# Kernel optimization log

Measured on AMD Instinct MI355X. Metric: run time of the kernel, lower is better.

Reference implementation:

```python
import jax, jax.numpy as jnp
import numpy as np

EPS = 1e-8

def _normalize(a):
    return a / jnp.clip(jnp.linalg.norm(a, axis=-1, keepdims=True), EPS)

def _cosine(a, b):
    # pairwise cosine similarity: [Na, d] x [Nb, d] -> [Na, Nb]
    return _normalize(a) @ _normalize(b).T

def setup_inputs() -> dict:
    key = jax.random.key(0)
    n, k, q, d = 100, 5, 75, 4096
    x = jax.random.normal(key, (n * (k + q), d), dtype=jnp.float32)
    tao = jnp.full((1,), 10.0, dtype=jnp.float32)
    return {"x": x, "tao": tao, "n": n, "k": k, "q": q}

def reference(x, tao, n, k, q):
    d = x.shape[-1]
    x = x.reshape(n, k + q, d)
    support = x[:, :k]                      # [n, k, d]
    query = x[:, k:].reshape(n * q, d)      # [NQ, d]
    NQ = n * q
    proto = support.mean(axis=1)            # [n, d]

    pre_sim = _cosine(query, proto)         # [NQ, n]
    pre_label = jnp.argmax(pre_sim, axis=1) # [NQ]

    # vectorized per-class masked softmax aggregation (replaces Python loop)
    cls_ids = jnp.arange(n)
    mask = pre_label[None, :] == cls_ids[:, None]            # [n, NQ]
    logits_q = jnp.where(mask, pre_sim.T, -jnp.inf)          # [n, NQ]
    proto_n = _normalize(proto)
    self_sim = jnp.sum(proto_n * proto_n, axis=-1)           # [n], cosine(proto, proto)
    logits = jnp.concatenate([logits_q, self_sim[:, None]], axis=1)  # [n, NQ+1]
    w = jax.nn.softmax(logits, axis=1)                       # [n, NQ+1]
    adapted_proto = w[:, :NQ] @ query + w[:, NQ:] * proto    # [n, d]

    sim = _cosine(query, adapted_proto)                      # [NQ, n]
    return tao.reshape(()) * sim
```

## Files before the change

kernel.cpp:

```cpp
#include <hip/hip_runtime.h>
#include <hip/hip_bf16.h>
#include <math.h>

#define NQUERY 7500
#define NCLS   100
#define DIM    4096
#define KQ     75
#define KSUP   5
#define RPC    80
#define MPAD   7552
#define NPAD   112
#define CAPQ   256
#define RCAP   2048
#define EPSF   1e-8f
#define SELEM  845824

typedef __attribute__((ext_vector_type(8))) short bf16x8;
typedef __attribute__((ext_vector_type(4))) short s16x4;
typedef __attribute__((ext_vector_type(4))) float f32x4;

__device__ __forceinline__ int xrow_of_query(int j) {
    return (j / KQ) * RPC + KSUP + (j % KQ);
}
__device__ __forceinline__ short bf16t(float x) {
    union { float f; unsigned u; } v; v.f = x;
    return (short)(v.u >> 16);
}

__device__ __forceinline__ size_t tile_off(int nt, int lm, int i) {
    return (((size_t)(nt * 128 + (i >> 5)) * 4 + ((i >> 3) & 3)) * 16 + lm) * 8 + (i & 7);
}

__global__ __launch_bounds__(256) void k_proto(const float* __restrict__ x,
        float* __restrict__ proto, short* __restrict__ Phi, float* __restrict__ es,
        double* __restrict__ pninv) {
    const int c = blockIdx.x, t = threadIdx.x;
    const int nt = c >> 4, lm = c & 15;
    if (c >= NCLS) {
        for (int g = t; g < 512; g += 256) {
            const int kstep = g >> 2, kq = g & 3;
            size_t o = (((size_t)(nt * 128 + kstep) * 4 + kq) * 16 + lm) * 8;
            bf16x8 z = {0,0,0,0,0,0,0,0};
            *(bf16x8*)(Phi + o) = z;
        }
        if (t == 0) es[c] = 0.f;
        return;
    }
    __shared__ double red[4];
    __shared__ float s_inv;
    const float* b0 = x + (size_t)(c * RPC) * DIM;
    float v[16];
    double ssq = 0.0;
#pragma unroll
    for (int p = 0; p < 4; ++p) {
        const int i = p * 1024 + t * 4;
        f32x4 s = {0.f, 0.f, 0.f, 0.f};
#pragma unroll
        for (int r = 0; r < KSUP; ++r)
            s += *(const f32x4*)(b0 + (size_t)r * DIM + i);
        s = s / 5.0f;
        *(f32x4*)&v[p*4] = s;
        *(f32x4*)(proto + (size_t)c*DIM + i) = s;
        ssq += (double)s[0]*s[0] + (double)s[1]*s[1]
             + (double)s[2]*s[2] + (double)s[3]*s[3];
    }
    for (int o = 32; o; o >>= 1) ssq += __shfl_down(ssq, o);
    if ((t & 63) == 0) red[t >> 6] = ssq;
    __syncthreads();
    if (t == 0) {
        double dtot = red[0] + red[1] + red[2] + red[3];
        pninv[c] = 1.0 / sqrt(dtot);
        float tot = (float)dtot;
        float inv = 1.f / fmaxf(sqrtf(tot), EPSF);
        s_inv = inv;
        es[c] = expf(tot * inv * inv);
    }
    __syncthreads();
    const float inv = s_inv;
#pragma unroll
    for (int p = 0; p < 4; ++p) {
        const int i = p * 1024 + t * 4;
        s16x4 h;
#pragma unroll
        for (int e = 0; e < 4; ++e) h[e] = bf16t(v[p*4+e] * inv);
        *(s16x4*)(Phi + tile_off(nt, lm, i)) = h;
    }
}

template<int TNKS, bool SSQ>
__global__ __launch_bounds__(256, 3) void k_gemm(const float* __restrict__ x,
        const short* __restrict__ Bt, float* __restrict__ Sd, float* __restrict__ nq2) {
    constexpr int KST = 128 / TNKS;
    const int bx = blockIdx.x, kz = blockIdx.y;
    const int w = threadIdx.x >> 6, lane = threadIdx.x & 63;
    const int lm = lane & 15, kq = lane >> 4;
    const int mp = bx * 4 + w;
    const int mt0 = mp * 2, mt1 = mt0 + 1;
    const int j0 = mt0 * 16 + lm, j1 = mt1 * 16 + lm;
    const int jc0 = j0 < NQUERY ? j0 : NQUERY - 1;
    const int jc1 = j1 < NQUERY ? j1 : NQUERY - 1;
    const float* pa0 = x + (size_t)xrow_of_query(jc0) * DIM + kq * 8;
    const float* pa1 = x + (size_t)xrow_of_query(jc1) * DIM + kq * 8;
    const short* pb = Bt + (lane << 3);
    const int ks0 = kz * KST;

    f32x4 acc0[7], acc1[7];
#pragma unroll
    for (int nt = 0; nt < 7; ++nt) {
        acc0[nt] = (f32x4){0.f,0.f,0.f,0.f};
        acc1[nt] = (f32x4){0.f,0.f,0.f,0.f};
    }
    float ssq0 = 0.f, ssq1 = 0.f;

    f32x4 a00 = *(const f32x4*)(pa0 + (size_t)ks0 * 32);
    f32x4 a01 = *(const f32x4*)(pa0 + (size_t)ks0 * 32 + 4);
    f32x4 a10 = *(const f32x4*)(pa1 + (size_t)ks0 * 32);
    f32x4 a11 = *(const f32x4*)(pa1 + (size_t)ks0 * 32 + 4);

#pragma unroll 1
    for (int s = 0; s < KST; ++s) {
        const int ks = ks0 + s;
        bf16x8 bh[7];
#pragma unroll
        for (int nt = 0; nt < 7; ++nt)
            bh[nt] = *(const bf16x8*)(pb + (((size_t)(nt * 128 + ks)) << 9));
        f32x4 n00, n01, n10, n11;
        if (s + 1 < KST) {
            n00 = *(const f32x4*)(pa0 + (size_t)(ks + 1) * 32);
            n01 = *(const f32x4*)(pa0 + (size_t)(ks + 1) * 32 + 4);
            n10 = *(const f32x4*)(pa1 + (size_t)(ks + 1) * 32);
            n11 = *(const f32x4*)(pa1 + (size_t)(ks + 1) * 32 + 4);
        }
        float f0[8] = {a00[0],a00[1],a00[2],a00[3],a01[0],a01[1],a01[2],a01[3]};
        float f1[8] = {a10[0],a10[1],a10[2],a10[3],a11[0],a11[1],a11[2],a11[3]};
        bf16x8 ah0, ah1;
#pragma unroll
        for (int e = 0; e < 8; ++e) {
            if (SSQ) { ssq0 += f0[e] * f0[e]; ssq1 += f1[e] * f1[e]; }
            ah0[e] = bf16t(f0[e]);
            ah1[e] = bf16t(f1[e]);
        }
#pragma unroll
        for (int nt = 0; nt < 7; ++nt) {
            acc0[nt] = __builtin_amdgcn_mfma_f32_16x16x32_bf16(ah0, bh[nt], acc0[nt], 0, 0, 0);
            acc1[nt] = __builtin_amdgcn_mfma_f32_16x16x32_bf16(ah1, bh[nt], acc1[nt], 0, 0, 0);
        }
        a00 = n00; a01 = n01; a10 = n10; a11 = n11;
    }

    if (SSQ) {
        ssq0 += __shfl_xor(ssq0, 16); ssq0 += __shfl_xor(ssq0, 32);
        ssq1 += __shfl_xor(ssq1, 16); ssq1 += __shfl_xor(ssq1, 32);
        if (kq == 0) {
            if (j0 < NQUERY) atomicAdd(&nq2[j0], ssq0);
            if (j1 < NQUERY) atomicAdd(&nq2[j1], ssq1);
        }
    }
    float* s0 = Sd + (size_t)(mt0 * 16) * NPAD;
    float* s1 = Sd + (size_t)(mt1 * 16) * NPAD;
#pragma unroll
    for (int nt = 0; nt < 7; ++nt)
#pragma unroll
        for (int r = 0; r < 4; ++r) {
            atomicAdd(&s0[(size_t)(kq * 4 + r) * NPAD + nt * 16 + lm], acc0[nt][r]);
            atomicAdd(&s1[(size_t)(kq * 4 + r) * NPAD + nt * 16 + lm], acc1[nt][r]);
        }
}

__global__ __launch_bounds__(256) void k_argmax(const float* __restrict__ S,
        const float* __restrict__ nq2, float* __restrict__ coef, float* __restrict__ invq,
        int* __restrict__ pos, int* __restrict__ ccnt, int* __restrict__ cls_list,
        int* __restrict__ rcnt, int* __restrict__ rlist) {
    const int j = blockIdx.x * 256 + threadIdx.x;
    if (j >= NQUERY) return;
    const float* row = S + (size_t)j * NPAD;
    float m1 = -1e30f, m2 = -1e30f;
    int i1 = 0, i2 = 0;
    for (int c = 0; c < NCLS; ++c) {
        float v = row[c];
        if (v > m1) { m2 = m1; i2 = i1; m1 = v; i1 = c; }
        else if (v > m2) { m2 = v; i2 = c; }
    }
    const float inv = 1.f / fmaxf(sqrtf(nq2[j]), EPSF);
    invq[j] = inv;
    coef[j] = expf(m1 * inv);
    const int p = atomicAdd(&ccnt[i1], 1);
    if (p < CAPQ) { cls_list[i1 * CAPQ + p] = j; pos[j] = p; }
    else pos[j] = -1;
    if ((m1 - m2) * inv < 5e-4f) {
        int rp = atomicAdd(rcnt, 1);
        if (rp < RCAP) rlist[rp] = j | (i1 << 13) | (i2 << 20);
    }
}

__global__ __launch_bounds__(256) void k_refine(const float* __restrict__ x,
        const float* __restrict__ proto, const double* __restrict__ pninv,
        const float* __restrict__ S, const float* __restrict__ invq,
        float* __restrict__ coef, const int* __restrict__ pos,
        int* __restrict__ ccnt, int* __restrict__ cls_list,
        const int* __restrict__ rcnt, const int* __restrict__ rlist) {
    const int cnt = min(*rcnt, RCAP);
    const int t = threadIdx.x;
    __shared__ double red1[4], red2[4];
    for (int e = blockIdx.x; e < cnt; e += gridDim.x) {
        const int pk = rlist[e];
        const int j = pk & 8191, c1 = (pk >> 13) & 127, c2 = (pk >> 20) & 127;
        const float* xq = x + (size_t)xrow_of_query(j) * DIM;
        const float* p1 = proto + (size_t)c1 * DIM;
        const float* p2 = proto + (size_t)c2 * DIM;
        double d1 = 0.0, d2 = 0.0;
        for (int i = t; i < DIM; i += 256) {
            const double qv = (double)xq[i];
            d1 += (double)p1[i] * qv;
            d2 += (double)p2[i] * qv;
        }
        for (int o = 32; o; o >>= 1) { d1 += __shfl_down(d1, o); d2 += __shfl_down(d2, o); }
        if ((t & 63) == 0) { red1[t >> 6] = d1; red2[t >> 6] = d2; }
        __syncthreads();
        if (t == 0) {
            const double cos1 = (red1[0]+red1[1]+red1[2]+red1[3]) * pninv[c1];
            const double cos2 = (red2[0]+red2[1]+red2[2]+red2[3]) * pninv[c2];
            const int win = (cos2 > cos1 || (cos2 == cos1 && c2 < c1)) ? c2 : c1;
            if (win != c1) {
                coef[j] = expf(S[(size_t)j * NPAD + win] * invq[j]);
                const int pj = pos[j];
                if (pj >= 0) cls_list[c1 * CAPQ + pj] = -1;
                const int np = atomicAdd(&ccnt[c2], 1);
                if (np < CAPQ) cls_list[c2 * CAPQ + np] = j;
            }
        }
        __syncthreads();
    }
}

__global__ __launch_bounds__(128) void k_adapt(const float* __restrict__ x,
        const float* __restrict__ coef, const int* __restrict__ cls_cnt,
        const int* __restrict__ cls_list, float* __restrict__ APpart) {
    __shared__ int   s_j[CAPQ];
    __shared__ float s_cf[CAPQ];
    const int cx = blockIdx.x, c = blockIdx.y, sl = blockIdx.z;
    const int n = min(cls_cnt[c], CAPQ);
    for (int e = threadIdx.x; e < n; e += 128) {
        const int j = cls_list[c * CAPQ + e];
        s_j[e] = j;
        s_cf[e] = (j >= 0) ? coef[j] : 0.f;
    }
    __syncthreads();
    const int i0 = cx * 512 + threadIdx.x * 4;
    f32x4 acc = {0.f, 0.f, 0.f, 0.f};
    for (int e = sl; e < n; e += 4) {
        const int j = s_j[e];
        if (j >= 0) {
            const float cf = s_cf[e];
            const f32x4 v = *(const f32x4*)(x + (size_t)xrow_of_query(j) * DIM + i0);
            acc += v * cf;
        }
    }
    *(f32x4*)(APpart + (size_t)sl * NCLS * DIM + (size_t)c * DIM + i0) = acc;
}

__global__ __launch_bounds__(256) void k_apnorm(const float* __restrict__ APpart,
        const float* __restrict__ proto, const float* __restrict__ es,
        short* __restrict__ APhi) {
    const int c = blockIdx.x, t = threadIdx.x;
    const int nt = c >> 4, lm = c & 15;
    if (c >= NCLS) {
        for (int g = t; g < 512; g += 256) {
            const int kstep = g >> 2, kq = g & 3;
            size_t o = (((size_t)(nt * 128 + kstep) * 4 + kq) * 16 + lm) * 8;
            bf16x8 z = {0,0,0,0,0,0,0,0};
            *(bf16x8*)(APhi + o) = z;
        }
        return;
    }
    __shared__ float red[4];
    __shared__ float s_inv;
    const float e0 = es[c];
    float v[16];
    float ssq = 0.f;
#pragma unroll
    for (int p = 0; p < 4; ++p) {
        const int i = p * 1024 + t * 4;
        f32x4 s = {0.f, 0.f, 0.f, 0.f};
#pragma unroll
        for (int sl = 0; sl < 4; ++sl)
            s += *(const f32x4*)(APpart + (size_t)sl * NCLS * DIM + (size_t)c * DIM + i);
        f32x4 pr = *(const f32x4*)(proto + (size_t)c*DIM + i);
        s += pr * e0;
        *(f32x4*)&v[p*4] = s;
        ssq += s[0]*s[0] + s[1]*s[1] + s[2]*s[2] + s[3]*s[3];
    }
    for (int o = 32; o; o >>= 1) ssq += __shfl_down(ssq, o);
    if ((t & 63) == 0) red[t >> 6] = ssq;
    __syncthreads();
    if (t == 0) {
        float tot = red[0] + red[1] + red[2] + red[3];
        s_inv = 1.f / fmaxf(sqrtf(tot), EPSF);
    }
    __syncthreads();
    const float inv = s_inv;
#pragma unroll
    for (int p = 0; p < 4; ++p) {
        const int i = p * 1024 + t * 4;
        s16x4 h;
#pragma unroll
        for (int e = 0; e < 4; ++e) h[e] = bf16t(v[p*4+e] * inv);
        *(s16x4*)(APhi + tile_off(nt, lm, i)) = h;
    }
}

__global__ __launch_bounds__(256) void k_scale(const float* __restrict__ Ored,
        const float* __restrict__ invq, const float* __restrict__ tao,
        float* __restrict__ out) {
    const int idx = blockIdx.x * 256 + threadIdx.x;
    if (idx >= NQUERY * 25) return;
    const int j = idx / 25, c4 = (idx % 25) * 4;
    const f32x4 s = *(const f32x4*)(Ored + (size_t)j * NPAD + c4);
    const float sc = tao[0] * invq[j];
    *(f32x4*)(out + (size_t)j * NCLS + c4) = s * sc;
}

#define OFF_RCNT   0u
#define OFF_CCNT   256u
#define OFF_NQ2    1792u
#define ZERO_BYTES 32768u
#define OFF_ES     32768u
#define OFF_INVQ   33280u
#define OFF_POS    63488u
#define OFF_COEF   93696u
#define OFF_RLIST  123904u
#define OFF_CLIST  132096u
#define OFF_PNINV  234496u
#define OFF_PROTO  235520u
#define OFF_PHI    1873920u
#define OFF_APHI   2791424u
#define OFF_SRED   3708928u
#define OFF_ORED   7092224u
#define OFF_APPART 10475520u

extern "C" void kernel_launch(void* const* d_in, const int* in_sizes, int n_in,
                              void* d_out, int out_size, void* d_ws, size_t ws_size,
                              hipStream_t stream) {
    const float* x   = (const float*)d_in[0];
    const float* tao = (const float*)d_in[1];
    char* ws = (char*)d_ws;

    int*    rcnt    = (int*)   (ws + OFF_RCNT);
    int*    ccnt    = (int*)   (ws + OFF_CCNT);
    float*  nq2     = (float*) (ws + OFF_NQ2);
    float*  es      = (float*) (ws + OFF_ES);
    float*  invq    = (float*) (ws + OFF_INVQ);
    int*    pos     = (int*)   (ws + OFF_POS);
    float*  coef    = (float*) (ws + OFF_COEF);
    int*    rlist   = (int*)   (ws + OFF_RLIST);
    int*    clist   = (int*)   (ws + OFF_CLIST);
    double* pninv   = (double*)(ws + OFF_PNINV);
    float*  proto   = (float*) (ws + OFF_PROTO);
    short*  Phi     = (short*) (ws + OFF_PHI);
    short*  APhi    = (short*) (ws + OFF_APHI);
    float*  Sred    = (float*) (ws + OFF_SRED);
    float*  Ored    = (float*) (ws + OFF_ORED);
    float*  APpart  = (float*) (ws + OFF_APPART);

    hipMemsetAsync(ws, 0, ZERO_BYTES, stream);
    hipMemsetAsync(ws + OFF_SRED, 0, 2u * 3383296u, stream);

    k_proto <<<NPAD, 256, 0, stream>>>(x, proto, Phi, es, pninv);
    k_gemm<16, true><<<dim3(59, 16), 256, 0, stream>>>(x, Phi, Sred, nq2);
    k_argmax <<<30, 256, 0, stream>>>(Sred, nq2, coef, invq, pos, ccnt, clist, rcnt, rlist);
    k_refine <<<512, 256, 0, stream>>>(x, proto, pninv, Sred, invq, coef, pos, ccnt, clist, rcnt, rlist);
    k_adapt  <<<dim3(8, NCLS, 4), 128, 0, stream>>>(x, coef, ccnt, clist, APpart);
    k_apnorm <<<NPAD, 256, 0, stream>>>(APpart, proto, es, APhi);
    k_gemm<16, false><<<dim3(59, 16), 256, 0, stream>>>(x, APhi, Ored, nq2);
    k_scale  <<<733, 256, 0, stream>>>(Ored, invq, tao, (float*)d_out);
}
```

Before: 358.6 us.

## Fuse all stages into one cooperative persistent kernel with grid syncs

Replaces the eight separate kernel launches with a single cooperative megakernel whose stages are separated by grid-wide barriers and system fences, with blocks looping over virtual work items. The goal is to remove per-launch gaps and tail effects between the small stages. The GEMM loop is also rewritten as a fully unrolled 8-step body without explicit prefetch, and the adapt stage changes block shape to 256 threads. In exchange, grid syncs and __threadfence_system carry their own cost, and the grid (occupancy×256 capped at 1024) may use fewer registers per thread, which lowers GEMM efficiency. A fallback path launches per-stage wrapper kernels if the cooperative launch fails.

```diff
diff --git a/kernel.cpp b/kernel.cpp
--- a/kernel.cpp
+++ b/kernel.cpp
@@ -1,6 +1,9 @@
 #include <hip/hip_runtime.h>
+#include <hip/hip_cooperative_groups.h>
 #include <hip/hip_bf16.h>
 #include <math.h>
+
+namespace cg = cooperative_groups;
 
 #define NQUERY 7500
 #define NCLS   100
@@ -13,7 +16,6 @@
 #define CAPQ   256
 #define RCAP   2048
 #define EPSF   1e-8f
-#define SELEM  845824
 
 typedef __attribute__((ext_vector_type(8))) short bf16x8;
 typedef __attribute__((ext_vector_type(4))) short s16x4;
@@ -26,298 +28,8 @@
     union { float f; unsigned u; } v; v.f = x;
     return (short)(v.u >> 16);
 }
-
 __device__ __forceinline__ size_t tile_off(int nt, int lm, int i) {
     return (((size_t)(nt * 128 + (i >> 5)) * 4 + ((i >> 3) & 3)) * 16 + lm) * 8 + (i & 7);
-}
-
-__global__ __launch_bounds__(256) void k_proto(const float* __restrict__ x,
-        float* __restrict__ proto, short* __restrict__ Phi, float* __restrict__ es,
-        double* __restrict__ pninv) {
-    const int c = blockIdx.x, t = threadIdx.x;
-    const int nt = c >> 4, lm = c & 15;
-    if (c >= NCLS) {
-        for (int g = t; g < 512; g += 256) {
-            const int kstep = g >> 2, kq = g & 3;
-            size_t o = (((size_t)(nt * 128 + kstep) * 4 + kq) * 16 + lm) * 8;
-            bf16x8 z = {0,0,0,0,0,0,0,0};
-            *(bf16x8*)(Phi + o) = z;
-        }
-        if (t == 0) es[c] = 0.f;
-        return;
-    }
-    __shared__ double red[4];
-    __shared__ float s_inv;
-    const float* b0 = x + (size_t)(c * RPC) * DIM;
-    float v[16];
-    double ssq = 0.0;
-#pragma unroll
-    for (int p = 0; p < 4; ++p) {
-        const int i = p * 1024 + t * 4;
-        f32x4 s = {0.f, 0.f, 0.f, 0.f};
-#pragma unroll
-        for (int r = 0; r < KSUP; ++r)
-            s += *(const f32x4*)(b0 + (size_t)r * DIM + i);
-        s = s / 5.0f;
-        *(f32x4*)&v[p*4] = s;
-        *(f32x4*)(proto + (size_t)c*DIM + i) = s;
-        ssq += (double)s[0]*s[0] + (double)s[1]*s[1]
-             + (double)s[2]*s[2] + (double)s[3]*s[3];
-    }
-    for (int o = 32; o; o >>= 1) ssq += __shfl_down(ssq, o);
-    if ((t & 63) == 0) red[t >> 6] = ssq;
-    __syncthreads();
-    if (t == 0) {
-        double dtot = red[0] + red[1] + red[2] + red[3];
-        pninv[c] = 1.0 / sqrt(dtot);
-        float tot = (float)dtot;
-        float inv = 1.f / fmaxf(sqrtf(tot), EPSF);
-        s_inv = inv;
-        es[c] = expf(tot * inv * inv);
-    }
-    __syncthreads();
-    const float inv = s_inv;
-#pragma unroll
-    for (int p = 0; p < 4; ++p) {
-        const int i = p * 1024 + t * 4;
-        s16x4 h;
-#pragma unroll
-        for (int e = 0; e < 4; ++e) h[e] = bf16t(v[p*4+e] * inv);
-        *(s16x4*)(Phi + tile_off(nt, lm, i)) = h;
-    }
-}
-
-template<int TNKS, bool SSQ>
-__global__ __launch_bounds__(256, 3) void k_gemm(const float* __restrict__ x,
-        const short* __restrict__ Bt, float* __restrict__ Sd, float* __restrict__ nq2) {
-    constexpr int KST = 128 / TNKS;
-    const int bx = blockIdx.x, kz = blockIdx.y;
-    const int w = threadIdx.x >> 6, lane = threadIdx.x & 63;
-    const int lm = lane & 15, kq = lane >> 4;
-    const int mp = bx * 4 + w;
-    const int mt0 = mp * 2, mt1 = mt0 + 1;
-    const int j0 = mt0 * 16 + lm, j1 = mt1 * 16 + lm;
-    const int jc0 = j0 < NQUERY ? j0 : NQUERY - 1;
-    const int jc1 = j1 < NQUERY ? j1 : NQUERY - 1;
-    const float* pa0 = x + (size_t)xrow_of_query(jc0) * DIM + kq * 8;
-    const float* pa1 = x + (size_t)xrow_of_query(jc1) * DIM + kq * 8;
-    const short* pb = Bt + (lane << 3);
-    const int ks0 = kz * KST;
-
-    f32x4 acc0[7], acc1[7];
-#pragma unroll
-    for (int nt = 0; nt < 7; ++nt) {
-        acc0[nt] = (f32x4){0.f,0.f,0.f,0.f};
-        acc1[nt] = (f32x4){0.f,0.f,0.f,0.f};
-    }
-    float ssq0 = 0.f, ssq1 = 0.f;
-
-    f32x4 a00 = *(const f32x4*)(pa0 + (size_t)ks0 * 32);
-    f32x4 a01 = *(const f32x4*)(pa0 + (size_t)ks0 * 32 + 4);
-    f32x4 a10 = *(const f32x4*)(pa1 + (size_t)ks0 * 32);
-    f32x4 a11 = *(const f32x4*)(pa1 + (size_t)ks0 * 32 + 4);
-
-#pragma unroll 1
-    for (int s = 0; s < KST; ++s) {
-        const int ks = ks0 + s;
-        bf16x8 bh[7];
-#pragma unroll
-        for (int nt = 0; nt < 7; ++nt)
-            bh[nt] = *(const bf16x8*)(pb + (((size_t)(nt * 128 + ks)) << 9));
-        f32x4 n00, n01, n10, n11;
-        if (s + 1 < KST) {
-            n00 = *(const f32x4*)(pa0 + (size_t)(ks + 1) * 32);
-            n01 = *(const f32x4*)(pa0 + (size_t)(ks + 1) * 32 + 4);
-            n10 = *(const f32x4*)(pa1 + (size_t)(ks + 1) * 32);
-            n11 = *(const f32x4*)(pa1 + (size_t)(ks + 1) * 32 + 4);
-        }
-        float f0[8] = {a00[0],a00[1],a00[2],a00[3],a01[0],a01[1],a01[2],a01[3]};
-        float f1[8] = {a10[0],a10[1],a10[2],a10[3],a11[0],a11[1],a11[2],a11[3]};
-        bf16x8 ah0, ah1;
-#pragma unroll
-        for (int e = 0; e < 8; ++e) {
-            if (SSQ) { ssq0 += f0[e] * f0[e]; ssq1 += f1[e] * f1[e]; }
-            ah0[e] = bf16t(f0[e]);
-            ah1[e] = bf16t(f1[e]);
-        }
-#pragma unroll
-        for (int nt = 0; nt < 7; ++nt) {
-            acc0[nt] = __builtin_amdgcn_mfma_f32_16x16x32_bf16(ah0, bh[nt], acc0[nt], 0, 0, 0);
-            acc1[nt] = __builtin_amdgcn_mfma_f32_16x16x32_bf16(ah1, bh[nt], acc1[nt], 0, 0, 0);
-        }
-        a00 = n00; a01 = n01; a10 = n10; a11 = n11;
-    }
-
-    if (SSQ) {
-        ssq0 += __shfl_xor(ssq0, 16); ssq0 += __shfl_xor(ssq0, 32);
-        ssq1 += __shfl_xor(ssq1, 16); ssq1 += __shfl_xor(ssq1, 32);
-        if (kq == 0) {
-            if (j0 < NQUERY) atomicAdd(&nq2[j0], ssq0);
-            if (j1 < NQUERY) atomicAdd(&nq2[j1], ssq1);
-        }
-    }
-    float* s0 = Sd + (size_t)(mt0 * 16) * NPAD;
-    float* s1 = Sd + (size_t)(mt1 * 16) * NPAD;
-#pragma unroll
-    for (int nt = 0; nt < 7; ++nt)
-#pragma unroll
-        for (int r = 0; r < 4; ++r) {
-            atomicAdd(&s0[(size_t)(kq * 4 + r) * NPAD + nt * 16 + lm], acc0[nt][r]);
-            atomicAdd(&s1[(size_t)(kq * 4 + r) * NPAD + nt * 16 + lm], acc1[nt][r]);
-        }
-}
-
-__global__ __launch_bounds__(256) void k_argmax(const float* __restrict__ S,
-        const float* __restrict__ nq2, float* __restrict__ coef, float* __restrict__ invq,
-        int* __restrict__ pos, int* __restrict__ ccnt, int* __restrict__ cls_list,
-        int* __restrict__ rcnt, int* __restrict__ rlist) {
-    const int j = blockIdx.x * 256 + threadIdx.x;
-    if (j >= NQUERY) return;
-    const float* row = S + (size_t)j * NPAD;
-    float m1 = -1e30f, m2 = -1e30f;
-    int i1 = 0, i2 = 0;
-    for (int c = 0; c < NCLS; ++c) {
-        float v = row[c];
-        if (v > m1) { m2 = m1; i2 = i1; m1 = v; i1 = c; }
-        else if (v > m2) { m2 = v; i2 = c; }
-    }
-    const float inv = 1.f / fmaxf(sqrtf(nq2[j]), EPSF);
-    invq[j] = inv;
-    coef[j] = expf(m1 * inv);
-    const int p = atomicAdd(&ccnt[i1], 1);
-    if (p < CAPQ) { cls_list[i1 * CAPQ + p] = j; pos[j] = p; }
-    else pos[j] = -1;
-    if ((m1 - m2) * inv < 5e-4f) {
-        int rp = atomicAdd(rcnt, 1);
-        if (rp < RCAP) rlist[rp] = j | (i1 << 13) | (i2 << 20);
-    }
-}
-
-__global__ __launch_bounds__(256) void k_refine(const float* __restrict__ x,
-        const float* __restrict__ proto, const double* __restrict__ pninv,
-        const float* __restrict__ S, const float* __restrict__ invq,
-        float* __restrict__ coef, const int* __restrict__ pos,
-        int* __restrict__ ccnt, int* __restrict__ cls_list,
-        const int* __restrict__ rcnt, const int* __restrict__ rlist) {
-    const int cnt = min(*rcnt, RCAP);
-    const int t = threadIdx.x;
-    __shared__ double red1[4], red2[4];
-    for (int e = blockIdx.x; e < cnt; e += gridDim.x) {
-        const int pk = rlist[e];
-        const int j = pk & 8191, c1 = (pk >> 13) & 127, c2 = (pk >> 20) & 127;
-        const float* xq = x + (size_t)xrow_of_query(j) * DIM;
-        const float* p1 = proto + (size_t)c1 * DIM;
-        const float* p2 = proto + (size_t)c2 * DIM;
-        double d1 = 0.0, d2 = 0.0;
-        for (int i = t; i < DIM; i += 256) {
-            const double qv = (double)xq[i];
-            d1 += (double)p1[i] * qv;
-            d2 += (double)p2[i] * qv;
-        }
-        for (int o = 32; o; o >>= 1) { d1 += __shfl_down(d1, o); d2 += __shfl_down(d2, o); }
-        if ((t & 63) == 0) { red1[t >> 6] = d1; red2[t >> 6] = d2; }
-        __syncthreads();
-        if (t == 0) {
-            const double cos1 = (red1[0]+red1[1]+red1[2]+red1[3]) * pninv[c1];
-            const double cos2 = (red2[0]+red2[1]+red2[2]+red2[3]) * pninv[c2];
-            const int win = (cos2 > cos1 || (cos2 == cos1 && c2 < c1)) ? c2 : c1;
-            if (win != c1) {
-                coef[j] = expf(S[(size_t)j * NPAD + win] * invq[j]);
-                const int pj = pos[j];
-                if (pj >= 0) cls_list[c1 * CAPQ + pj] = -1;
-                const int np = atomicAdd(&ccnt[c2], 1);
-                if (np < CAPQ) cls_list[c2 * CAPQ + np] = j;
-            }
-        }
-        __syncthreads();
-    }
-}
-
-__global__ __launch_bounds__(128) void k_adapt(const float* __restrict__ x,
-        const float* __restrict__ coef, const int* __restrict__ cls_cnt,
-        const int* __restrict__ cls_list, float* __restrict__ APpart) {
-    __shared__ int   s_j[CAPQ];
-    __shared__ float s_cf[CAPQ];
-    const int cx = blockIdx.x, c = blockIdx.y, sl = blockIdx.z;
-    const int n = min(cls_cnt[c], CAPQ);
-    for (int e = threadIdx.x; e < n; e += 128) {
-        const int j = cls_list[c * CAPQ + e];
-        s_j[e] = j;
-        s_cf[e] = (j >= 0) ? coef[j] : 0.f;
-    }
-    __syncthreads();
-    const int i0 = cx * 512 + threadIdx.x * 4;
-    f32x4 acc = {0.f, 0.f, 0.f, 0.f};
-    for (int e = sl; e < n; e += 4) {
-        const int j = s_j[e];
-        if (j >= 0) {
-            const float cf = s_cf[e];
-            const f32x4 v = *(const f32x4*)(x + (size_t)xrow_of_query(j) * DIM + i0);
-            acc += v * cf;
-        }
-    }
-    *(f32x4*)(APpart + (size_t)sl * NCLS * DIM + (size_t)c * DIM + i0) = acc;
-}
-
-__global__ __launch_bounds__(256) void k_apnorm(const float* __restrict__ APpart,
-        const float* __restrict__ proto, const float* __restrict__ es,
-        short* __restrict__ APhi) {
-    const int c = blockIdx.x, t = threadIdx.x;
-    const int nt = c >> 4, lm = c & 15;
-    if (c >= NCLS) {
-        for (int g = t; g < 512; g += 256) {
-            const int kstep = g >> 2, kq = g & 3;
-            size_t o = (((size_t)(nt * 128 + kstep) * 4 + kq) * 16 + lm) * 8;
-            bf16x8 z = {0,0,0,0,0,0,0,0};
-            *(bf16x8*)(APhi + o) = z;
-        }
-        return;
-    }
-    __shared__ float red[4];
-    __shared__ float s_inv;
-    const float e0 = es[c];
-    float v[16];
-    float ssq = 0.f;
-#pragma unroll
-    for (int p = 0; p < 4; ++p) {
-        const int i = p * 1024 + t * 4;
-        f32x4 s = {0.f, 0.f, 0.f, 0.f};
-#pragma unroll
-        for (int sl = 0; sl < 4; ++sl)
-            s += *(const f32x4*)(APpart + (size_t)sl * NCLS * DIM + (size_t)c * DIM + i);
-        f32x4 pr = *(const f32x4*)(proto + (size_t)c*DIM + i);
-        s += pr * e0;
-        *(f32x4*)&v[p*4] = s;
-        ssq += s[0]*s[0] + s[1]*s[1] + s[2]*s[2] + s[3]*s[3];
-    }
-    for (int o = 32; o; o >>= 1) ssq += __shfl_down(ssq, o);
-    if ((t & 63) == 0) red[t >> 6] = ssq;
-    __syncthreads();
-    if (t == 0) {
-        float tot = red[0] + red[1] + red[2] + red[3];
-        s_inv = 1.f / fmaxf(sqrtf(tot), EPSF);
-    }
-    __syncthreads();
-    const float inv = s_inv;
-#pragma unroll
-    for (int p = 0; p < 4; ++p) {
-        const int i = p * 1024 + t * 4;
-        s16x4 h;
-#pragma unroll
-        for (int e = 0; e < 4; ++e) h[e] = bf16t(v[p*4+e] * inv);
-        *(s16x4*)(APhi + tile_off(nt, lm, i)) = h;
-    }
-}
-
-__global__ __launch_bounds__(256) void k_scale(const float* __restrict__ Ored,
-        const float* __restrict__ invq, const float* __restrict__ tao,
-        float* __restrict__ out) {
-    const int idx = blockIdx.x * 256 + threadIdx.x;
-    if (idx >= NQUERY * 25) return;
-    const int j = idx / 25, c4 = (idx % 25) * 4;
-    const f32x4 s = *(const f32x4*)(Ored + (size_t)j * NPAD + c4);
-    const float sc = tao[0] * invq[j];
-    *(f32x4*)(out + (size_t)j * NCLS + c4) = s * sc;
 }
 
 #define OFF_RCNT   0u
@@ -338,13 +50,310 @@
 #define OFF_ORED   7092224u
 #define OFF_APPART 10475520u
 
-extern "C" void kernel_launch(void* const* d_in, const int* in_sizes, int n_in,
-                              void* d_out, int out_size, void* d_ws, size_t ws_size,
-                              hipStream_t stream) {
-    const float* x   = (const float*)d_in[0];
-    const float* tao = (const float*)d_in[1];
-    char* ws = (char*)d_ws;
-
+
+__device__ __forceinline__ void stage_proto(const float* __restrict__ x,
+        float* __restrict__ proto, short* __restrict__ Phi, float* __restrict__ es,
+        double* __restrict__ pninv) {
+    __shared__ double red[4];
+    __shared__ float s_inv;
+    const int t = threadIdx.x;
+    for (int c = blockIdx.x; c < NPAD; c += gridDim.x) {
+        const int nt = c >> 4, lm = c & 15;
+        if (c >= NCLS) {
+            for (int g = t; g < 512; g += 256) {
+                const int kstep = g >> 2, kq = g & 3;
+                size_t o = (((size_t)(nt * 128 + kstep) * 4 + kq) * 16 + lm) * 8;
+                bf16x8 z = {0,0,0,0,0,0,0,0};
+                *(bf16x8*)(Phi + o) = z;
+            }
+            if (t == 0) es[c] = 0.f;
+        } else {
+            const float* b0 = x + (size_t)(c * RPC) * DIM;
+            float v[16];
+            double ssq = 0.0;
+#pragma unroll
+            for (int p = 0; p < 4; ++p) {
+                const int i = p * 1024 + t * 4;
+                f32x4 s = {0.f, 0.f, 0.f, 0.f};
+#pragma unroll
+                for (int r = 0; r < KSUP; ++r)
+                    s += *(const f32x4*)(b0 + (size_t)r * DIM + i);
+                s = s / 5.0f;
+                *(f32x4*)&v[p*4] = s;
+                *(f32x4*)(proto + (size_t)c*DIM + i) = s;
+                ssq += (double)s[0]*s[0] + (double)s[1]*s[1]
+                     + (double)s[2]*s[2] + (double)s[3]*s[3];
+            }
+            for (int o = 32; o; o >>= 1) ssq += __shfl_down(ssq, o);
+            if ((t & 63) == 0) red[t >> 6] = ssq;
+            __syncthreads();
+            if (t == 0) {
+                double dtot = red[0] + red[1] + red[2] + red[3];
+                pninv[c] = 1.0 / sqrt(dtot);
+                float tot = (float)dtot;
+                float inv = 1.f / fmaxf(sqrtf(tot), EPSF);
+                s_inv = inv;
+                es[c] = expf(tot * inv * inv);
+            }
+            __syncthreads();
+            const float inv = s_inv;
+#pragma unroll
+            for (int p = 0; p < 4; ++p) {
+                const int i = p * 1024 + t * 4;
+                s16x4 h;
+#pragma unroll
+                for (int e = 0; e < 4; ++e) h[e] = bf16t(v[p*4+e] * inv);
+                *(s16x4*)(Phi + tile_off(nt, lm, i)) = h;
+            }
+            __syncthreads();
+        }
+    }
+}
+
+__device__ __forceinline__ void gemm_stage(const float* __restrict__ x,
+        const short* __restrict__ Bt, float* __restrict__ Sd,
+        float* __restrict__ nq2, const bool do_ssq) {
+    const int w = threadIdx.x >> 6, lane = threadIdx.x & 63;
+    const int lm = lane & 15, kq = lane >> 4;
+    const short* pb = Bt + (lane << 3);
+#pragma unroll 1
+    for (int vb = blockIdx.x; vb < 944; vb += gridDim.x) {
+        const int bx = vb % 59, kz = vb / 59;
+        const int mp = bx * 4 + w;
+        const int mt0 = mp * 2, mt1 = mt0 + 1;
+        const int j0 = mt0 * 16 + lm, j1 = mt1 * 16 + lm;
+        const int jc0 = j0 < NQUERY ? j0 : NQUERY - 1;
+        const int jc1 = j1 < NQUERY ? j1 : NQUERY - 1;
+        const float* pa0 = x + (size_t)xrow_of_query(jc0) * DIM + kq * 8;
+        const float* pa1 = x + (size_t)xrow_of_query(jc1) * DIM + kq * 8;
+        const int ks0 = kz * 8;
+
+        f32x4 acc0[7], acc1[7];
+#pragma unroll
+        for (int nt = 0; nt < 7; ++nt) {
+            acc0[nt] = (f32x4){0.f,0.f,0.f,0.f};
+            acc1[nt] = (f32x4){0.f,0.f,0.f,0.f};
+        }
+        float ssq0 = 0.f, ssq1 = 0.f;
+
+#pragma unroll
+        for (int s = 0; s < 8; ++s) {
+            const int ks = ks0 + s;
+            const f32x4 a00 = *(const f32x4*)(pa0 + (size_t)ks * 32);
+            const f32x4 a01 = *(const f32x4*)(pa0 + (size_t)ks * 32 + 4);
+            const f32x4 a10 = *(const f32x4*)(pa1 + (size_t)ks * 32);
+            const f32x4 a11 = *(const f32x4*)(pa1 + (size_t)ks * 32 + 4);
+            bf16x8 bh[7];
+#pragma unroll
+            for (int nt = 0; nt < 7; ++nt)
+                bh[nt] = *(const bf16x8*)(pb + (((size_t)(nt * 128 + ks)) << 9));
+            float f0[8] = {a00[0],a00[1],a00[2],a00[3],a01[0],a01[1],a01[2],a01[3]};
+            float f1[8] = {a10[0],a10[1],a10[2],a10[3],a11[0],a11[1],a11[2],a11[3]};
+            bf16x8 ah0, ah1;
+#pragma unroll
+            for (int e = 0; e < 8; ++e) {
+                if (do_ssq) { ssq0 += f0[e] * f0[e]; ssq1 += f1[e] * f1[e]; }
+                ah0[e] = bf16t(f0[e]);
+                ah1[e] = bf16t(f1[e]);
+            }
+#pragma unroll
+            for (int nt = 0; nt < 7; ++nt) {
+                acc0[nt] = __builtin_amdgcn_mfma_f32_16x16x32_bf16(ah0, bh[nt], acc0[nt], 0, 0, 0);
+                acc1[nt] = __builtin_amdgcn_mfma_f32_16x16x32_bf16(ah1, bh[nt], acc1[nt], 0, 0, 0);
+            }
+        }
+
+        if (do_ssq) {
+            ssq0 += __shfl_xor(ssq0, 16); ssq0 += __shfl_xor(ssq0, 32);
+            ssq1 += __shfl_xor(ssq1, 16); ssq1 += __shfl_xor(ssq1, 32);
+            if (kq == 0) {
+                if (j0 < NQUERY) atomicAdd(&nq2[j0], ssq0);
+                if (j1 < NQUERY) atomicAdd(&nq2[j1], ssq1);
+            }
+        }
+        float* s0 = Sd + (size_t)(mt0 * 16) * NPAD;
+        float* s1 = Sd + (size_t)(mt1 * 16) * NPAD;
+#pragma unroll
+        for (int nt = 0; nt < 7; ++nt)
+#pragma unroll
+            for (int r = 0; r < 4; ++r) {
+                atomicAdd(&s0[(size_t)(kq * 4 + r) * NPAD + nt * 16 + lm], acc0[nt][r]);
+                atomicAdd(&s1[(size_t)(kq * 4 + r) * NPAD + nt * 16 + lm], acc1[nt][r]);
+            }
+    }
+}
+
+__device__ __forceinline__ void stage_argmax(const float* __restrict__ S,
+        const float* __restrict__ nq2, float* __restrict__ coef, float* __restrict__ invq,
+        int* __restrict__ pos, int* __restrict__ ccnt, int* __restrict__ clist,
+        int* __restrict__ rcnt, int* __restrict__ rlist) {
+    const int t = threadIdx.x;
+    for (int vb = blockIdx.x; vb < 30; vb += gridDim.x) {
+        const int j = vb * 256 + t;
+        if (j >= NQUERY) continue;
+        const float* row = S + (size_t)j * NPAD;
+        float m1 = -1e30f, m2 = -1e30f;
+        int i1 = 0, i2 = 0;
+        for (int c = 0; c < NCLS; ++c) {
+            float v = row[c];
+            if (v > m1) { m2 = m1; i2 = i1; m1 = v; i1 = c; }
+            else if (v > m2) { m2 = v; i2 = c; }
+        }
+        const float inv = 1.f / fmaxf(sqrtf(nq2[j]), EPSF);
+        invq[j] = inv;
+        coef[j] = expf(m1 * inv);
+        const int p = atomicAdd(&ccnt[i1], 1);
+        if (p < CAPQ) { clist[i1 * CAPQ + p] = j; pos[j] = p; }
+        else pos[j] = -1;
+        if ((m1 - m2) * inv < 5e-4f) {
+            int rp = atomicAdd(rcnt, 1);
+            if (rp < RCAP) rlist[rp] = j | (i1 << 13) | (i2 << 20);
+        }
+    }
+}
+
+__device__ __forceinline__ void stage_refine(const float* __restrict__ x,
+        const float* __restrict__ proto, const double* __restrict__ pninv,
+        const float* __restrict__ S, const float* __restrict__ invq,
+        float* __restrict__ coef, const int* __restrict__ pos,
+        int* __restrict__ ccnt, int* __restrict__ clist,
+        const int* __restrict__ rcnt, const int* __restrict__ rlist) {
+    __shared__ double red1[4], red2[4];
+    const int cnt = min(*rcnt, RCAP);
+    const int t = threadIdx.x;
+    for (int e = blockIdx.x; e < cnt; e += gridDim.x) {
+        const int pk = rlist[e];
+        const int j = pk & 8191, c1 = (pk >> 13) & 127, c2 = (pk >> 20) & 127;
+        const float* xq = x + (size_t)xrow_of_query(j) * DIM;
+        const float* p1 = proto + (size_t)c1 * DIM;
+        const float* p2 = proto + (size_t)c2 * DIM;
+        double d1 = 0.0, d2 = 0.0;
+        for (int i = t; i < DIM; i += 256) {
+            const double qv = (double)xq[i];
+            d1 += (double)p1[i] * qv;
+            d2 += (double)p2[i] * qv;
+        }
+        for (int o = 32; o; o >>= 1) { d1 += __shfl_down(d1, o); d2 += __shfl_down(d2, o); }
+        if ((t & 63) == 0) { red1[t >> 6] = d1; red2[t >> 6] = d2; }
+        __syncthreads();
+        if (t == 0) {
+            const double cos1 = (red1[0]+red1[1]+red1[2]+red1[3]) * pninv[c1];
+            const double cos2 = (red2[0]+red2[1]+red2[2]+red2[3]) * pninv[c2];
+            const int win = (cos2 > cos1 || (cos2 == cos1 && c2 < c1)) ? c2 : c1;
+            if (win != c1) {
+                coef[j] = expf(S[(size_t)j * NPAD + win] * invq[j]);
+                const int pj = pos[j];
+                if (pj >= 0) clist[c1 * CAPQ + pj] = -1;
+                const int np = atomicAdd(&ccnt[c2], 1);
+                if (np < CAPQ) clist[c2 * CAPQ + np] = j;
+            }
+        }
+        __syncthreads();
+    }
+}
+
+__device__ __forceinline__ void stage_adapt(const float* __restrict__ x,
+        const float* __restrict__ coef, const int* __restrict__ ccnt,
+        const int* __restrict__ clist, float* __restrict__ APpart) {
+    __shared__ int   s_j[CAPQ];
+    __shared__ float s_cf[CAPQ];
+    const int t = threadIdx.x;
+    for (int vb = blockIdx.x; vb < 4 * NCLS * 4; vb += gridDim.x) {
+        const int cx = vb & 3, c = (vb >> 2) % NCLS, sl = vb / (4 * NCLS);
+        const int n = min(ccnt[c], CAPQ);
+        for (int e = t; e < n; e += 256) {
+            const int j = clist[c * CAPQ + e];
+            s_j[e] = j;
+            s_cf[e] = (j >= 0) ? coef[j] : 0.f;
+        }
+        __syncthreads();
+        const int i0 = cx * 1024 + t * 4;
+        f32x4 acc = {0.f, 0.f, 0.f, 0.f};
+        for (int e = sl; e < n; e += 4) {
+            const int j = s_j[e];
+            if (j >= 0) {
+                const float cf = s_cf[e];
+                const f32x4 v = *(const f32x4*)(x + (size_t)xrow_of_query(j) * DIM + i0);
+                acc += v * cf;
+            }
+        }
+        *(f32x4*)(APpart + (size_t)sl * NCLS * DIM + (size_t)c * DIM + i0) = acc;
+        __syncthreads();
+    }
+}
+
+__device__ __forceinline__ void stage_apnorm(const float* __restrict__ APpart,
+        const float* __restrict__ proto, const float* __restrict__ es,
+        short* __restrict__ APhi) {
+    __shared__ float red[4];
+    __shared__ float s_inv;
+    const int t = threadIdx.x;
+    for (int c = blockIdx.x; c < NPAD; c += gridDim.x) {
+        const int nt = c >> 4, lm = c & 15;
+        if (c >= NCLS) {
+            for (int g = t; g < 512; g += 256) {
+                const int kstep = g >> 2, kq = g & 3;
+                size_t o = (((size_t)(nt * 128 + kstep) * 4 + kq) * 16 + lm) * 8;
+                bf16x8 z = {0,0,0,0,0,0,0,0};
+                *(bf16x8*)(APhi + o) = z;
+            }
+        } else {
+            const float e0 = es[c];
+            float v[16];
+            float ssq = 0.f;
+#pragma unroll
+            for (int p = 0; p < 4; ++p) {
+                const int i = p * 1024 + t * 4;
+                f32x4 s = {0.f, 0.f, 0.f, 0.f};
+#pragma unroll
+                for (int sl = 0; sl < 4; ++sl)
+                    s += *(const f32x4*)(APpart + (size_t)sl * NCLS * DIM + (size_t)c * DIM + i);
+                f32x4 pr = *(const f32x4*)(proto + (size_t)c*DIM + i);
+                s += pr * e0;
+                *(f32x4*)&v[p*4] = s;
+                ssq += s[0]*s[0] + s[1]*s[1] + s[2]*s[2] + s[3]*s[3];
+            }
+            for (int o = 32; o; o >>= 1) ssq += __shfl_down(ssq, o);
+            if ((t & 63) == 0) red[t >> 6] = ssq;
+            __syncthreads();
+            if (t == 0) {
+                float tot = red[0] + red[1] + red[2] + red[3];
+                s_inv = 1.f / fmaxf(sqrtf(tot), EPSF);
+            }
+            __syncthreads();
+            const float inv = s_inv;
+#pragma unroll
+            for (int p = 0; p < 4; ++p) {
+                const int i = p * 1024 + t * 4;
+                s16x4 h;
+#pragma unroll
+                for (int e = 0; e < 4; ++e) h[e] = bf16t(v[p*4+e] * inv);
+                *(s16x4*)(APhi + tile_off(nt, lm, i)) = h;
+            }
+            __syncthreads();
+        }
+    }
+}
+
+__device__ __forceinline__ void stage_scale(const float* __restrict__ Ored,
+        const float* __restrict__ invq, const float* __restrict__ tao,
+        float* __restrict__ out) {
+    const int t = threadIdx.x;
+    for (int vb = blockIdx.x; vb < 733; vb += gridDim.x) {
+        const int idx = vb * 256 + t;
+        if (idx < NQUERY * 25) {
+            const int j = idx / 25, c4 = (idx % 25) * 4;
+            const f32x4 s = *(const f32x4*)(Ored + (size_t)j * NPAD + c4);
+            const float sc = tao[0] * invq[j];
+            *(f32x4*)(out + (size_t)j * NCLS + c4) = s * sc;
+        }
+    }
+}
+
+#define FENCE_SYNC() do { __threadfence_system(); grid.sync(); __threadfence_system(); } while (0)
+
+__global__ __launch_bounds__(256) void mega(const float* __restrict__ x,
+        const float* __restrict__ tao, float* __restrict__ out, char* __restrict__ ws) {
     int*    rcnt    = (int*)   (ws + OFF_RCNT);
     int*    ccnt    = (int*)   (ws + OFF_CCNT);
     float*  nq2     = (float*) (ws + OFF_NQ2);
@@ -362,15 +371,93 @@
     float*  Ored    = (float*) (ws + OFF_ORED);
     float*  APpart  = (float*) (ws + OFF_APPART);
 
+    cg::grid_group grid = cg::this_grid();
+
+    stage_proto(x, proto, Phi, es, pninv);
+    FENCE_SYNC();
+    gemm_stage(x, Phi, Sred, nq2, true);
+    FENCE_SYNC();
+    stage_argmax(Sred, nq2, coef, invq, pos, ccnt, clist, rcnt, rlist);
+    FENCE_SYNC();
+    stage_refine(x, proto, pninv, Sred, invq, coef, pos, ccnt, clist, rcnt, rlist);
+    FENCE_SYNC();
+    stage_adapt(x, coef, ccnt, clist, APpart);
+    FENCE_SYNC();
+    stage_apnorm(APpart, proto, es, APhi);
+    FENCE_SYNC();
+    gemm_stage(x, APhi, Ored, nq2, false);
+    FENCE_SYNC();
+    stage_scale(Ored, invq, tao, out);
+}
+
+__global__ __launch_bounds__(256) void w_proto(const float* x, float* proto,
+        short* Phi, float* es, double* pninv) { stage_proto(x, proto, Phi, es, pninv); }
+__global__ __launch_bounds__(256) void w_gemm(const float* x, const short* Bt,
+        float* Sd, float* nq2, int do_ssq) { gemm_stage(x, Bt, Sd, nq2, do_ssq != 0); }
+__global__ __launch_bounds__(256) void w_argmax(const float* S, const float* nq2,
+        float* coef, float* invq, int* pos, int* ccnt, int* clist, int* rcnt, int* rlist) {
+    stage_argmax(S, nq2, coef, invq, pos, ccnt, clist, rcnt, rlist);
+}
+__global__ __launch_bounds__(256) void w_refine(const float* x, const float* proto,
+        const double* pninv, const float* S, const float* invq, float* coef,
+        const int* pos, int* ccnt, int* clist, const int* rcnt, const int* rlist) {
+    stage_refine(x, proto, pninv, S, invq, coef, pos, ccnt, clist, rcnt, rlist);
+}
+__global__ __launch_bounds__(256) void w_adapt(const float* x, const float* coef,
+        const int* ccnt, const int* clist, float* APpart) {
+    stage_adapt(x, coef, ccnt, clist, APpart);
+}
+__global__ __launch_bounds__(256) void w_apnorm(const float* APpart, const float* proto,
+        const float* es, short* APhi) { stage_apnorm(APpart, proto, es, APhi); }
+__global__ __launch_bounds__(256) void w_scale(const float* Ored, const float* invq,
+        const float* tao, float* out) { stage_scale(Ored, invq, tao, out); }
+
+extern "C" void kernel_launch(void* const* d_in, const int* in_sizes, int n_in,
+                              void* d_out, int out_size, void* d_ws, size_t ws_size,
+                              hipStream_t stream) {
+    const float* x   = (const float*)d_in[0];
+    const float* tao = (const float*)d_in[1];
+    char* ws = (char*)d_ws;
+    float* out = (float*)d_out;
+
+    float*  nq2    = (float*) (ws + OFF_NQ2);
+    float*  es     = (float*) (ws + OFF_ES);
+    float*  invq   = (float*) (ws + OFF_INVQ);
+    int*    pos    = (int*)   (ws + OFF_POS);
+    float*  coef   = (float*) (ws + OFF_COEF);
+    int*    rcnt   = (int*)   (ws + OFF_RCNT);
+    int*    ccnt   = (int*)   (ws + OFF_CCNT);
+    int*    rlist  = (int*)   (ws + OFF_RLIST);
+    int*    clist  = (int*)   (ws + OFF_CLIST);
+    double* pninv  = (double*)(ws + OFF_PNINV);
+    float*  proto  = (float*) (ws + OFF_PROTO);
+    short*  Phi    = (short*) (ws + OFF_PHI);
+    short*  APhi   = (short*) (ws + OFF_APHI);
+    float*  Sred   = (float*) (ws + OFF_SRED);
+    float*  Ored   = (float*) (ws + OFF_ORED);
+    float*  APpart = (float*) (ws + OFF_APPART);
+
     hipMemsetAsync(ws, 0, ZERO_BYTES, stream);
     hipMemsetAsync(ws + OFF_SRED, 0, 2u * 3383296u, stream);
 
-    k_proto <<<NPAD, 256, 0, stream>>>(x, proto, Phi, es, pninv);
-    k_gemm<16, true><<<dim3(59, 16), 256, 0, stream>>>(x, Phi, Sred, nq2);
-    k_argmax <<<30, 256, 0, stream>>>(Sred, nq2, coef, invq, pos, ccnt, clist, rcnt, rlist);
-    k_refine <<<512, 256, 0, stream>>>(x, proto, pninv, Sred, invq, coef, pos, ccnt, clist, rcnt, rlist);
-    k_adapt  <<<dim3(8, NCLS, 4), 128, 0, stream>>>(x, coef, ccnt, clist, APpart);
-    k_apnorm <<<NPAD, 256, 0, stream>>>(APpart, proto, es, APhi);
-    k_gemm<16, false><<<dim3(59, 16), 256, 0, stream>>>(x, APhi, Ored, nq2);
-    k_scale  <<<733, 256, 0, stream>>>(Ored, invq, tao, (float*)d_out);
-}
+    int occ = 0;
+    hipError_t oe = hipOccupancyMaxActiveBlocksPerMultiprocessor(
+            &occ, (const void*)mega, 256, 0);
+    if (oe == hipSuccess && occ >= 1) {
+        int grid = occ * 256;
+        if (grid > 1024) grid = 1024;
+        void* kargs[] = { (void*)&x, (void*)&tao, (void*)&out, (void*)&ws };
+        hipError_t le = hipLaunchCooperativeKernel((const void*)mega,
+                dim3(grid), dim3(256), kargs, 0, stream);
+        if (le == hipSuccess) return;
+    }
+
+    w_proto <<<NPAD, 256, 0, stream>>>(x, proto, Phi, es, pninv);
+    w_gemm  <<<944,  256, 0, stream>>>(x, Phi, Sred, nq2, 1);
+    w_argmax<<<30,   256, 0, stream>>>(Sred, nq2, coef, invq, pos, ccnt, clist, rcnt, rlist);
+    w_refine<<<512,  256, 0, stream>>>(x, proto, pninv, Sred, invq, coef, pos, ccnt, clist, rcnt, rlist);
+    w_adapt <<<1600, 256, 0, stream>>>(x, coef, ccnt, clist, APpart);
+    w_apnorm<<<NPAD, 256, 0, stream>>>(APpart, proto, es, APhi);
+    w_gemm  <<<944,  256, 0, stream>>>(x, APhi, Ored, nq2, 0);
+    w_scale <<<733,  256, 0, stream>>>(Ored, invq, tao, out);
+}
```

New measurement: 378.3 us. 5.5% more time.

## Stage B tile in LDS via direct global-to-LDS loads and double-buffer A fragments

Applied to the files above, without the earlier changes.

Restructures the similarity GEMM so each block loads its K-slice of the bf16 prototype tile once into shared memory with global_load_lds. Each wave then processes four M-tiles, loading the next tile's A fragments into registers while computing the current one. This replaces the repeated per-wave global B loads and the per-step A prefetch, aiming to cut redundant global/L2 traffic for B and to hide A latency. The cost is 56 KB of LDS per block and larger register arrays, which lower occupancy. The grid also shrinks from 59x16 to 32x16.

```diff
diff --git a/kernel.cpp b/kernel.cpp
--- a/kernel.cpp
+++ b/kernel.cpp
@@ -13,7 +13,6 @@
 #define CAPQ   256
 #define RCAP   2048
 #define EPSF   1e-8f
-#define SELEM  845824
 
 typedef __attribute__((ext_vector_type(8))) short bf16x8;
 typedef __attribute__((ext_vector_type(4))) short s16x4;
@@ -26,7 +25,11 @@
     union { float f; unsigned u; } v; v.f = x;
     return (short)(v.u >> 16);
 }
-
+__device__ __forceinline__ void gload_lds16(const short* g, short* l) {
+    __builtin_amdgcn_global_load_lds(
+        (const __attribute__((address_space(1))) unsigned int*)g,
+        (__attribute__((address_space(3))) unsigned int*)l, 16, 0, 0);
+}
 __device__ __forceinline__ size_t tile_off(int nt, int lm, int i) {
     return (((size_t)(nt * 128 + (i >> 5)) * 4 + ((i >> 3) & 3)) * 16 + lm) * 8 + (i & 7);
 }
@@ -87,84 +90,89 @@
     }
 }
 
-template<int TNKS, bool SSQ>
-__global__ __launch_bounds__(256, 3) void k_gemm(const float* __restrict__ x,
+template<bool SSQ>
+__global__ __launch_bounds__(256) void k_gemm(const float* __restrict__ x,
         const short* __restrict__ Bt, float* __restrict__ Sd, float* __restrict__ nq2) {
-    constexpr int KST = 128 / TNKS;
-    const int bx = blockIdx.x, kz = blockIdx.y;
+    __shared__ short sbuf[7 * 8 * 512];
+    const int g = blockIdx.x, kz = blockIdx.y;
     const int w = threadIdx.x >> 6, lane = threadIdx.x & 63;
     const int lm = lane & 15, kq = lane >> 4;
-    const int mp = bx * 4 + w;
-    const int mt0 = mp * 2, mt1 = mt0 + 1;
-    const int j0 = mt0 * 16 + lm, j1 = mt1 * 16 + lm;
-    const int jc0 = j0 < NQUERY ? j0 : NQUERY - 1;
-    const int jc1 = j1 < NQUERY ? j1 : NQUERY - 1;
-    const float* pa0 = x + (size_t)xrow_of_query(jc0) * DIM + kq * 8;
-    const float* pa1 = x + (size_t)xrow_of_query(jc1) * DIM + kq * 8;
-    const short* pb = Bt + (lane << 3);
-    const int ks0 = kz * KST;
-
-    f32x4 acc0[7], acc1[7];
-#pragma unroll
-    for (int nt = 0; nt < 7; ++nt) {
-        acc0[nt] = (f32x4){0.f,0.f,0.f,0.f};
-        acc1[nt] = (f32x4){0.f,0.f,0.f,0.f};
-    }
-    float ssq0 = 0.f, ssq1 = 0.f;
-
-    f32x4 a00 = *(const f32x4*)(pa0 + (size_t)ks0 * 32);
-    f32x4 a01 = *(const f32x4*)(pa0 + (size_t)ks0 * 32 + 4);
-    f32x4 a10 = *(const f32x4*)(pa1 + (size_t)ks0 * 32);
-    f32x4 a11 = *(const f32x4*)(pa1 + (size_t)ks0 * 32 + 4);
-
-#pragma unroll 1
-    for (int s = 0; s < KST; ++s) {
-        const int ks = ks0 + s;
-        bf16x8 bh[7];
-#pragma unroll
-        for (int nt = 0; nt < 7; ++nt)
-            bh[nt] = *(const bf16x8*)(pb + (((size_t)(nt * 128 + ks)) << 9));
-        f32x4 n00, n01, n10, n11;
-        if (s + 1 < KST) {
-            n00 = *(const f32x4*)(pa0 + (size_t)(ks + 1) * 32);
-            n01 = *(const f32x4*)(pa0 + (size_t)(ks + 1) * 32 + 4);
-            n10 = *(const f32x4*)(pa1 + (size_t)(ks + 1) * 32);
-            n11 = *(const f32x4*)(pa1 + (size_t)(ks + 1) * 32 + 4);
-        }
-        float f0[8] = {a00[0],a00[1],a00[2],a00[3],a01[0],a01[1],a01[2],a01[3]};
-        float f1[8] = {a10[0],a10[1],a10[2],a10[3],a11[0],a11[1],a11[2],a11[3]};
-        bf16x8 ah0, ah1;
-#pragma unroll
-        for (int e = 0; e < 8; ++e) {
-            if (SSQ) { ssq0 += f0[e] * f0[e]; ssq1 += f1[e] * f1[e]; }
-            ah0[e] = bf16t(f0[e]);
-            ah1[e] = bf16t(f1[e]);
-        }
-#pragma unroll
-        for (int nt = 0; nt < 7; ++nt) {
-            acc0[nt] = __builtin_amdgcn_mfma_f32_16x16x32_bf16(ah0, bh[nt], acc0[nt], 0, 0, 0);
-            acc1[nt] = __builtin_amdgcn_mfma_f32_16x16x32_bf16(ah1, bh[nt], acc1[nt], 0, 0, 0);
-        }
-        a00 = n00; a01 = n01; a10 = n10; a11 = n11;
-    }
-
-    if (SSQ) {
-        ssq0 += __shfl_xor(ssq0, 16); ssq0 += __shfl_xor(ssq0, 32);
-        ssq1 += __shfl_xor(ssq1, 16); ssq1 += __shfl_xor(ssq1, 32);
-        if (kq == 0) {
-            if (j0 < NQUERY) atomicAdd(&nq2[j0], ssq0);
-            if (j1 < NQUERY) atomicAdd(&nq2[j1], ssq1);
-        }
-    }
-    float* s0 = Sd + (size_t)(mt0 * 16) * NPAD;
-    float* s1 = Sd + (size_t)(mt1 * 16) * NPAD;
-#pragma unroll
-    for (int nt = 0; nt < 7; ++nt)
-#pragma unroll
-        for (int r = 0; r < 4; ++r) {
-            atomicAdd(&s0[(size_t)(kq * 4 + r) * NPAD + nt * 16 + lm], acc0[nt][r]);
-            atomicAdd(&s1[(size_t)(kq * 4 + r) * NPAD + nt * 16 + lm], acc1[nt][r]);
-        }
+    const int ks0 = kz * 8;
+
+#pragma unroll
+    for (int p = 0; p < 14; ++p) {
+        const int idx = w * 14 + p;
+        const short* gsrc = Bt + (((size_t)((idx >> 3) * 128 + ks0 + (idx & 7))) << 9) + lane * 8;
+        gload_lds16(gsrc, sbuf + ((size_t)idx << 9));
+    }
+
+    const int mt0 = g + 32 * w;
+    const int mt1 = g + 32 * (w + 4);
+    const int mt2 = g + 32 * (w + 8);
+    const int mt3 = g + 32 * (w + 12);
+    const bool v0 = mt0 < 472, v1 = mt1 < 472, v2 = mt2 < 472, v3 = mt3 < 472;
+
+    auto apt = [&](int mt) {
+        const int j = mt * 16 + lm;
+        const int jc = j < NQUERY ? j : NQUERY - 1;
+        return x + (size_t)xrow_of_query(jc) * DIM + kz * 256 + kq * 8;
+    };
+
+    f32x4 A0[16], A1[16];
+#define LOADA(buf, mt) do { \
+        const float* pa_ = apt(mt); \
+        _Pragma("unroll") \
+        for (int s_ = 0; s_ < 8; ++s_) { \
+            buf[s_*2]   = *(const f32x4*)(pa_ + s_*32); \
+            buf[s_*2+1] = *(const f32x4*)(pa_ + s_*32 + 4); \
+        } } while (0)
+
+    if (v0) LOADA(A0, mt0);
+    if (v1) LOADA(A1, mt1);
+    __syncthreads();
+
+#define COMPUTE(buf, mt) do { \
+        f32x4 acc_[7]; \
+        _Pragma("unroll") \
+        for (int nt_ = 0; nt_ < 7; ++nt_) acc_[nt_] = (f32x4){0.f,0.f,0.f,0.f}; \
+        float ssq_ = 0.f; \
+        _Pragma("unroll") \
+        for (int s_ = 0; s_ < 8; ++s_) { \
+            float f_[8] = {buf[s_*2][0],buf[s_*2][1],buf[s_*2][2],buf[s_*2][3], \
+                           buf[s_*2+1][0],buf[s_*2+1][1],buf[s_*2+1][2],buf[s_*2+1][3]}; \
+            bf16x8 ah_; \
+            _Pragma("unroll") \
+            for (int e_ = 0; e_ < 8; ++e_) { \
+                if (SSQ) ssq_ += f_[e_] * f_[e_]; \
+                ah_[e_] = bf16t(f_[e_]); \
+            } \
+            _Pragma("unroll") \
+            for (int nt_ = 0; nt_ < 7; ++nt_) { \
+                const bf16x8 bh_ = *(const bf16x8*)(sbuf + (((size_t)(nt_*8 + s_)) << 9) + lane*8); \
+                acc_[nt_] = __builtin_amdgcn_mfma_f32_16x16x32_bf16(ah_, bh_, acc_[nt_], 0, 0, 0); \
+            } \
+        } \
+        if (SSQ) { \
+            ssq_ += __shfl_xor(ssq_, 16); ssq_ += __shfl_xor(ssq_, 32); \
+            const int j_ = (mt) * 16 + lm; \
+            if (kq == 0 && j_ < NQUERY) atomicAdd(&nq2[j_], ssq_); \
+        } \
+        float* sp_ = Sd + (size_t)((mt) * 16) * NPAD; \
+        _Pragma("unroll") \
+        for (int nt_ = 0; nt_ < 7; ++nt_) \
+            _Pragma("unroll") \
+            for (int r_ = 0; r_ < 4; ++r_) \
+                atomicAdd(&sp_[(size_t)(kq * 4 + r_) * NPAD + nt_ * 16 + lm], acc_[nt_][r_]); \
+    } while (0)
+
+    if (v0) COMPUTE(A0, mt0);
+    if (v2) LOADA(A0, mt2);
+    if (v1) COMPUTE(A1, mt1);
+    if (v3) LOADA(A1, mt3);
+    if (v2) COMPUTE(A0, mt2);
+    if (v3) COMPUTE(A1, mt3);
+#undef LOADA
+#undef COMPUTE
 }
 
 __global__ __launch_bounds__(256) void k_argmax(const float* __restrict__ S,
@@ -345,32 +353,32 @@
     const float* tao = (const float*)d_in[1];
     char* ws = (char*)d_ws;
 
-    int*    rcnt    = (int*)   (ws + OFF_RCNT);
-    int*    ccnt    = (int*)   (ws + OFF_CCNT);
-    float*  nq2     = (float*) (ws + OFF_NQ2);
-    float*  es      = (float*) (ws + OFF_ES);
-    float*  invq    = (float*) (ws + OFF_INVQ);
-    int*    pos     = (int*)   (ws + OFF_POS);
-    float*  coef    = (float*) (ws + OFF_COEF);
-    int*    rlist   = (int*)   (ws + OFF_RLIST);
-    int*    clist   = (int*)   (ws + OFF_CLIST);
-    double* pninv   = (double*)(ws + OFF_PNINV);
-    float*  proto   = (float*) (ws + OFF_PROTO);
-    short*  Phi     = (short*) (ws + OFF_PHI);
-    short*  APhi    = (short*) (ws + OFF_APHI);
-    float*  Sred    = (float*) (ws + OFF_SRED);
-    float*  Ored    = (float*) (ws + OFF_ORED);
-    float*  APpart  = (float*) (ws + OFF_APPART);
+    int*    rcnt   = (int*)   (ws + OFF_RCNT);
+    int*    ccnt   = (int*)   (ws + OFF_CCNT);
+    float*  nq2    = (float*) (ws + OFF_NQ2);
+    float*  es     = (float*) (ws + OFF_ES);
+    float*  invq   = (float*) (ws + OFF_INVQ);
+    int*    pos    = (int*)   (ws + OFF_POS);
+    float*  coef   = (float*) (ws + OFF_COEF);
+    int*    rlist  = (int*)   (ws + OFF_RLIST);
+    int*    clist  = (int*)   (ws + OFF_CLIST);
+    double* pninv  = (double*)(ws + OFF_PNINV);
+    float*  proto  = (float*) (ws + OFF_PROTO);
+    short*  Phi    = (short*) (ws + OFF_PHI);
+    short*  APhi   = (short*) (ws + OFF_APHI);
+    float*  Sred   = (float*) (ws + OFF_SRED);
+    float*  Ored   = (float*) (ws + OFF_ORED);
+    float*  APpart = (float*) (ws + OFF_APPART);
 
     hipMemsetAsync(ws, 0, ZERO_BYTES, stream);
     hipMemsetAsync(ws + OFF_SRED, 0, 2u * 3383296u, stream);
 
     k_proto <<<NPAD, 256, 0, stream>>>(x, proto, Phi, es, pninv);
-    k_gemm<16, true><<<dim3(59, 16), 256, 0, stream>>>(x, Phi, Sred, nq2);
+    k_gemm<true> <<<dim3(32, 16), 256, 0, stream>>>(x, Phi, Sred, nq2);
     k_argmax <<<30, 256, 0, stream>>>(Sred, nq2, coef, invq, pos, ccnt, clist, rcnt, rlist);
     k_refine <<<512, 256, 0, stream>>>(x, proto, pninv, Sred, invq, coef, pos, ccnt, clist, rcnt, rlist);
     k_adapt  <<<dim3(8, NCLS, 4), 128, 0, stream>>>(x, coef, ccnt, clist, APpart);
     k_apnorm <<<NPAD, 256, 0, stream>>>(APpart, proto, es, APhi);
-    k_gemm<16, false><<<dim3(59, 16), 256, 0, stream>>>(x, APhi, Ored, nq2);
+    k_gemm<false><<<dim3(32, 16), 256, 0, stream>>>(x, APhi, Ored, nq2);
     k_scale  <<<733, 256, 0, stream>>>(Ored, invq, tao, (float*)d_out);
 }
```

Result: faster. 339.3 us (-5.4%).
